# Kernel optimization log

Hardware: AMD Instinct MI355X
Metric: run time of the kernel (lower is better)

## Reference

```python
import jax, jax.numpy as jnp
from jax import lax
import numpy as np
import math

B, LBL, PRED, CIN = 16, 48, 336, 7
L = LBL + PRED
DM, E = 512, 2
DIN, N, DCONV = 2 * DM, 16, 4
DTR = math.ceil(DM / 16)  # 32
TF = 4  # freq='h' time features
EPS = 1e-5


def _ln(x, w, b):
    m = x.mean(-1, keepdims=True)
    v = ((x - m) ** 2).mean(-1, keepdims=True)
    return (x - m) / jnp.sqrt(v + EPS) * w + b


def _silu(x):
    return x * jax.nn.sigmoid(x)


def _token_embed(x, w):
    # Conv1d(c_in, d_model, k=3, padding=1, circular, bias=False). x: (B,L,C), w: (DM,C,3)
    xp = jnp.concatenate([x[:, -1:], x, x[:, :1]], axis=1)  # circular pad along L
    y = lax.conv_general_dilated(xp.transpose(0, 2, 1), w, (1,), 'VALID',
                                 dimension_numbers=('NCH', 'OIH', 'NCH'))
    return y.transpose(0, 2, 1)  # (B,L,DM)


def _selective_scan(u, dt, A, Bm, Cm):
    # u,dt: (B,L,DIN); A: (DIN,N); Bm,Cm: (B,L,N)
    h0 = jnp.zeros((u.shape[0], DIN, N), u.dtype)

    def step(h, inp):
        u_t, dt_t, B_t, C_t = inp  # (B,DIN),(B,DIN),(B,N),(B,N)
        dA = jnp.exp(dt_t[:, :, None] * A)  # (B,DIN,N)
        h = dA * h + (dt_t * u_t)[:, :, None] * B_t[:, None, :]
        y = jnp.einsum('bdn,bn->bd', h, C_t)
        return h, y

    _, ys = lax.scan(step, h0, (u.transpose(1, 0, 2), dt.transpose(1, 0, 2),
                                Bm.transpose(1, 0, 2), Cm.transpose(1, 0, 2)))
    return ys.transpose(1, 0, 2)  # (B,L,DIN)


def _mamba(x, p):
    (in_w, conv_w, conv_b, xproj_w, dtproj_w, dtproj_b, A_log, Dp, out_w) = p
    xz = x @ in_w.T                      # (B,L,2*DIN)
    xin, z = jnp.split(xz, 2, axis=-1)
    # depthwise causal conv1d, kernel DCONV
    xt = jnp.pad(xin.transpose(0, 2, 1), ((0, 0), (0, 0), (DCONV - 1, 0)))
    xc = lax.conv_general_dilated(xt, conv_w, (1,), 'VALID', feature_group_count=DIN,
                                  dimension_numbers=('NCH', 'OIH', 'NCH'))
    xc = _silu((xc + conv_b[None, :, None]).transpose(0, 2, 1))  # (B,L,DIN)
    dbc = xc @ xproj_w.T                 # (B,L,DTR+2N)
    dt_r, Bm, Cm = dbc[..., :DTR], dbc[..., DTR:DTR + N], dbc[..., DTR + N:]
    dt = jax.nn.softplus(dt_r @ dtproj_w.T + dtproj_b)  # (B,L,DIN)
    A = -jnp.exp(A_log)                  # (DIN,N)
    y = _selective_scan(xc, dt, A, Bm, Cm) + xc * Dp
    y = y * _silu(z)
    return y @ out_w.T                   # (B,L,DM)


def _model(x_dec, x_mark_dec, token_w, timef_w, layer_ps, fin_w, fin_b, out_w):
    mean = lax.stop_gradient(x_dec[:, :LBL].mean(1, keepdims=True))
    head = x_dec[:, :LBL] - mean
    std = lax.stop_gradient(jnp.sqrt(head.var(axis=1, keepdims=True) + EPS))
    head = head / std
    xd = jnp.concatenate([head, x_dec[:, LBL:]], axis=1)
    x = _token_embed(xd, token_w) + x_mark_dec @ timef_w.T  # DataEmbedding_wo_pos (eval: no dropout)
    for i in range(E):
        nw, nb = layer_ps[0][i], layer_ps[1][i]
        mp = tuple(layer_ps[j][i] for j in range(2, 11))
        x = x + _mamba(_ln(x, nw, nb), mp)
    x = _ln(x, fin_w, fin_b)
    out = x @ out_w.T
    out = out * std + mean
    return out[:, -PRED:, :]


def setup_inputs() -> dict:
    key = jax.random.key(0)
    ks = jax.random.split(key, 20)
    s = 0.02
    d = {
        'x_enc': jax.random.normal(ks[0], (B, 96, CIN), jnp.float32),
        'x_mark_enc': jax.random.normal(ks[1], (B, 96, TF), jnp.float32),
        'x_dec': jax.random.normal(ks[2], (B, L, CIN), jnp.float32),
        'x_mark_dec': jax.random.normal(ks[3], (B, L, TF), jnp.float32),
        'token_w': jax.random.normal(ks[4], (DM, CIN, 3), jnp.float32) * s,
        'timef_w': jax.random.normal(ks[5], (DM, TF), jnp.float32) * s,
        'norm_w': jnp.ones((E, DM), jnp.float32),
        'norm_b': jnp.zeros((E, DM), jnp.float32),
        'in_proj_w': jax.random.normal(ks[6], (E, 2 * DIN, DM), jnp.float32) * s,
        'conv_w': jax.random.normal(ks[7], (E, DIN, 1, DCONV), jnp.float32) * s,
        'conv_b': jnp.zeros((E, DIN), jnp.float32),
        'xproj_w': jax.random.normal(ks[8], (E, DTR + 2 * N, DIN), jnp.float32) * s,
        'dtproj_w': jax.random.normal(ks[9], (E, DIN, DTR), jnp.float32) * s,
        'dtproj_b': jnp.full((E, DIN), -4.0, jnp.float32),
        'A_log': jnp.tile(jnp.log(jnp.arange(1, N + 1, dtype=jnp.float32)), (E, DIN, 1)),
        'D': jnp.ones((E, DIN), jnp.float32),
        'outproj_w': jax.random.normal(ks[10], (E, DM, DIN), jnp.float32) * s,
        'final_norm_w': jnp.ones((DM,), jnp.float32),
        'final_norm_b': jnp.zeros((DM,), jnp.float32),
        'out_w': jax.random.normal(ks[11], (CIN, DM), jnp.float32) * s,
    }
    return d


def reference(x_enc, x_mark_enc, x_dec, x_mark_dec, token_w, timef_w, norm_w, norm_b,
              in_proj_w, conv_w, conv_b, xproj_w, dtproj_w, dtproj_b, A_log, D,
              outproj_w, final_norm_w, final_norm_b, out_w):
    layer_ps = (norm_w, norm_b, in_proj_w, conv_w, conv_b, xproj_w, dtproj_w,
                dtproj_b, A_log, D, outproj_w)
    return _model(x_dec, x_mark_dec, token_w, timef_w, layer_ps,
                  final_norm_w, final_norm_b, out_w)
```

## Files before the change

### kernel.cpp

```cpp
#include <hip/hip_runtime.h>

#define B_    16
#define LBL_  48
#define PRED_ 336
#define CIN_  7
#define L_    384
#define DM_   512
#define E_    2
#define DIN_  1024
#define N_    16
#define DCONV_ 4
#define DTR_  32
#define TF_   4
#define EPSF  1e-5f
#define NSEG  16
#define SEGL  24
#define SC2   2
#define NCHK  12

typedef unsigned short u16;
typedef __attribute__((ext_vector_type(8))) short short8;
typedef __attribute__((ext_vector_type(4))) float f32x4;

__device__ __forceinline__ float bf2f(u16 u){
  union { float f; unsigned int i; } cv; cv.i = ((unsigned int)u) << 16; return cv.f;
}
__device__ __forceinline__ u16 f2bf(float f){
  union { float f; unsigned int i; } cv; cv.f = f;
  unsigned int x = cv.i;
  unsigned int lsb = (x >> 16) & 1u;
  x += 0x7fffu + lsb;
  return (u16)(x >> 16);
}
__device__ __forceinline__ float lo16(unsigned int v){
  union { float f; unsigned int i; } cv; cv.i = v << 16; return cv.f;
}
__device__ __forceinline__ float hi16(unsigned int v){
  union { float f; unsigned int i; } cv; cv.i = v & 0xffff0000u; return cv.f;
}

#define GLDS(g, l) __builtin_amdgcn_global_load_lds( \
    (const __attribute__((address_space(1))) void*)(g), \
    (__attribute__((address_space(3))) void*)(l), 16, 0, 0)

#define PO_XDEC   0
#define PO_XMARK  43008
#define PO_TOKW   67584
#define PO_TIMEF  78336
#define PO_NORMW  80384
#define PO_NORMB  81408
#define PO_INW    82432
#define PO_CONVW  2179584
#define PO_CONVB  2187776
#define PO_XPROJ  2189824
#define PO_DTW    2320896
#define PO_DTB    2386432
#define PO_ALOG   2388480
#define PO_DP     2421248
#define PO_OUTW   2423296
#define PO_FNW    3471872
#define PO_FNB    3472384
#define PO_HEADW  3472896
#define P_TOTAL   3476480
#define A_X    3476480
#define A_LNB  6622208
#define A_XZ   9767936
#define A_DT   22350848
#define A_DBC  28642304
#define A_XD   29035520
#define A_MEAN 29078528
#define A_STD  29078640
#define A_DTR  29100032

struct Ptrs { const void* p[18]; };

__device__ __forceinline__ float wredsum(float s){
  #pragma unroll
  for (int off = 32; off; off >>= 1) s += __shfl_xor(s, off, 64);
  return s;
}

__device__ __forceinline__ void qpowers(float q, float* p){
  float q2 = q*q;
  float q4 = q2*q2;
  float q8 = q4*q4;
  float q3 = q2*q;
  p[0]=q;      p[1]=q2;     p[2]=q3;     p[3]=q4;
  p[4]=q4*q;   p[5]=q4*q2;  p[6]=q4*q3;  p[7]=q8;
  p[8]=q8*q;   p[9]=q8*q2;  p[10]=q8*q3; p[11]=q8*q4;
  p[12]=q8*p[4]; p[13]=q8*p[5]; p[14]=q8*p[6]; p[15]=q8*q8;
}

__global__ __launch_bounds__(256) void convert_kernel(Ptrs ps, float* __restrict__ dst){
  const int offs[18] = {PO_XDEC, PO_XMARK, PO_TOKW, PO_TIMEF, PO_NORMW, PO_NORMB,
                        PO_INW, PO_CONVW, PO_CONVB, PO_XPROJ, PO_DTW, PO_DTB,
                        PO_ALOG, PO_DP, PO_OUTW, PO_FNW, PO_FNB, PO_HEADW};
  int idx = blockIdx.x * 256 + threadIdx.x;
  if (idx >= P_TOTAL) return;
  int seg = 0;
  #pragma unroll
  for (int s = 1; s < 18; s++) if (idx >= offs[s]) seg = s;
  int off = idx - offs[seg];
  int isbf = (((const u16*)ps.p[4])[0] == 0x3F80u);
  if (seg == 6 || seg == 9 || seg == 10 || seg == 14){
    u16 hv = isbf ? ((const u16*)ps.p[seg])[off]
                  : f2bf(((const float*)ps.p[seg])[off]);
    ((u16*)(dst + offs[seg]))[off] = hv;
  } else {
    float v = isbf ? bf2f(((const u16*)ps.p[seg])[off])
                   : ((const float*)ps.p[seg])[off];
    dst[idx] = v;
  }
}

__global__ __launch_bounds__(64) void prep_kernel(const float* __restrict__ x_dec, float* __restrict__ xd,
                            float* __restrict__ meanv, float* __restrict__ stdv){
  int i = blockIdx.x;
  int b = i / CIN_, c = i % CIN_;
  int lane = threadIdx.x;
  float v0 = (lane < LBL_) ? x_dec[(b*L_+lane)*CIN_+c] : 0.f;
  float m = wredsum(v0) * (1.f/LBL_);
  float dv = (lane < LBL_) ? (v0 - m) : 0.f;
  float sd = sqrtf(wredsum(dv*dv) * (1.f/LBL_) + EPSF);
  if (lane == 0){ meanv[i] = m; stdv[i] = sd; }
  float inv = 1.f / sd;
  #pragma unroll
  for (int t = lane; t < L_; t += 64){
    float v = x_dec[(b*L_+t)*CIN_+c];
    xd[(b*L_+t)*CIN_+c] = (t < LBL_) ? (v - m) * inv : v;
  }
}

__global__ __launch_bounds__(256) void embed_ln_kernel(const float* __restrict__ xd,
      const float* __restrict__ token_w, const float* __restrict__ x_mark,
      const float* __restrict__ timef_w, const float* __restrict__ nw,
      const float* __restrict__ nb, float* __restrict__ x, u16* __restrict__ out){
  int tok = blockIdx.x*4 + (threadIdx.x >> 6);
  int lane = threadIdx.x & 63;
  int t = tok % L_;
  int b = tok / L_;
  int tm1 = (t == 0) ? L_-1 : t-1;
  int tp1 = (t == L_-1) ? 0 : t+1;
  const float* r0 = xd + (b*L_+tm1)*CIN_;
  const float* r1 = xd + (b*L_+t  )*CIN_;
  const float* r2 = xd + (b*L_+tp1)*CIN_;
  const float* mk = x_mark + (b*L_+t)*TF_;
  float a0[CIN_], a1[CIN_], a2[CIN_], mkv[TF_];
  #pragma unroll
  for (int ci = 0; ci < CIN_; ci++){ a0[ci]=r0[ci]; a1[ci]=r1[ci]; a2[ci]=r2[ci]; }
  #pragma unroll
  for (int f = 0; f < TF_; f++) mkv[f] = mk[f];
  float v[8];
  #pragma unroll
  for (int j = 0; j < 8; j++){
    int d = lane*8 + j;
    float acc = 0.f;
    #pragma unroll
    for (int ci = 0; ci < CIN_; ci++){
      const float* w = token_w + (d*CIN_+ci)*3;
      acc += a0[ci]*w[0] + a1[ci]*w[1] + a2[ci]*w[2];
    }
    #pragma unroll
    for (int f = 0; f < TF_; f++)
      acc += mkv[f] * timef_w[d*TF_+f];
    v[j] = acc;
  }
  float* xr = x + (size_t)tok*DM_ + lane*8;
  *(float4*)xr       = (float4){v[0],v[1],v[2],v[3]};
  *(float4*)(xr + 4) = (float4){v[4],v[5],v[6],v[7]};
  float s = (v[0]+v[1])+(v[2]+v[3])+((v[4]+v[5])+(v[6]+v[7]));
  float mean = wredsum(s) * (1.f/DM_);
  float s2 = 0.f;
  #pragma unroll
  for (int j = 0; j < 8; j++){ v[j] -= mean; s2 += v[j]*v[j]; }
  float rstd = rsqrtf(wredsum(s2) * (1.f/DM_) + EPSF);
  const float* wr = nw + lane*8;
  const float* br = nb + lane*8;
  uint4 o; unsigned int* op = (unsigned int*)&o;
  #pragma unroll
  for (int k = 0; k < 4; k++){
    u16 e0 = f2bf(v[2*k]   * rstd * wr[2*k]   + br[2*k]);
    u16 e1 = f2bf(v[2*k+1] * rstd * wr[2*k+1] + br[2*k+1]);
    op[k] = (unsigned int)e0 | ((unsigned int)e1 << 16);
  }
  *(uint4*)(out + (size_t)tok*DM_ + lane*8) = o;
}

__global__ __launch_bounds__(256) void ln_kernel(const float* __restrict__ x,
     const float* __restrict__ w, const float* __restrict__ bias, u16* __restrict__ out){
  int tok = blockIdx.x*4 + (threadIdx.x >> 6);
  int lane = threadIdx.x & 63;
  const float* xr = x + (size_t)tok*DM_ + lane*8;
  float4 a = *(const float4*)xr;
  float4 bq = *(const float4*)(xr + 4);
  float v[8] = {a.x,a.y,a.z,a.w,bq.x,bq.y,bq.z,bq.w};
  float s = (v[0]+v[1])+(v[2]+v[3])+((v[4]+v[5])+(v[6]+v[7]));
  float mean = wredsum(s) * (1.f/DM_);
  float s2 = 0.f;
  #pragma unroll
  for (int j = 0; j < 8; j++){ v[j] -= mean; s2 += v[j]*v[j]; }
  float rstd = rsqrtf(wredsum(s2) * (1.f/DM_) + EPSF);
  const float* wr = w + lane*8;
  const float* br = bias + lane*8;
  uint4 o; unsigned int* op = (unsigned int*)&o;
  #pragma unroll
  for (int k = 0; k < 4; k++){
    u16 e0 = f2bf(v[2*k]   * rstd * wr[2*k]   + br[2*k]);
    u16 e1 = f2bf(v[2*k+1] * rstd * wr[2*k+1] + br[2*k+1]);
    op[k] = (unsigned int)e0 | ((unsigned int)e1 << 16);
  }
  *(uint4*)(out + (size_t)tok*DM_ + lane*8) = o;
}

template<int TN, int ACCUM, int BF16OUT, int DTR>
__global__ __launch_bounds__(256) void gemm_mfma(const u16* __restrict__ A, const u16* __restrict__ Wt,
    void* __restrict__ C, int M, int N, int K, u16* __restrict__ dtrb){
  constexpr int WN = TN / 2;
  constexpr int NI = WN / 16;
  __shared__ u16 As[128 * 32];
  __shared__ u16 Ws[TN * 32];
  int tid = threadIdx.x;
  int wv = tid >> 6, lane = tid & 63;
  int wm = (wv & 1) * 64, wn = (wv >> 1) * WN;
  int m0 = blockIdx.y * 128, n0 = blockIdx.x * TN;
  int la = lane & 15, lk = lane >> 4;
  f32x4 acc[4][NI];
  #pragma unroll
  for (int i = 0; i < 4; i++)
    #pragma unroll
    for (int j = 0; j < NI; j++) acc[i][j] = (f32x4){0.f, 0.f, 0.f, 0.f};
  int srow = lane >> 2, scol = (lane & 3) * 8;
  const u16* Ag0 = A + (size_t)(m0 + wv*32 + srow) * K + scol;
  const u16* Ag1 = Ag0 + (size_t)16 * K;
  u16* Al0 = As + wv*1024 + lane*8;
  u16* Al1 = As + wv*1024 + 512 + lane*8;
  const u16 *Wg0, *Wg1;
  u16 *Wl0, *Wl1;
  if constexpr (TN == 128){
    Wg0 = Wt + (size_t)(n0 + wv*32 + srow) * K + scol;
    Wg1 = Wg0 + (size_t)16 * K;
    Wl0 = Ws + wv*1024 + lane*8;
    Wl1 = Ws + wv*1024 + 512 + lane*8;
  } else {
    Wg0 = Wt + (size_t)(n0 + wv*16 + srow) * K + scol;
    Wg1 = nullptr;
    Wl0 = Ws + wv*512 + lane*8;
    Wl1 = nullptr;
  }
  for (int k0 = 0; k0 < K; k0 += 32){
    GLDS(Ag0 + k0, Al0);
    GLDS(Ag1 + k0, Al1);
    GLDS(Wg0 + k0, Wl0);
    if constexpr (TN == 128) GLDS(Wg1 + k0, Wl1);
    __syncthreads();
    short8 af[4], bfr[NI];
    #pragma unroll
    for (int mi = 0; mi < 4; mi++) af[mi] = *(const short8*)&As[(wm + mi*16 + la)*32 + lk*8];
    #pragma unroll
    for (int ni = 0; ni < NI; ni++) bfr[ni] = *(const short8*)&Ws[(wn + ni*16 + la)*32 + lk*8];
    #pragma unroll
    for (int mi = 0; mi < 4; mi++)
      #pragma unroll
      for (int ni = 0; ni < NI; ni++)
        acc[mi][ni] = __builtin_amdgcn_mfma_f32_16x16x32_bf16(af[mi], bfr[ni], acc[mi][ni], 0, 0, 0);
    __syncthreads();
  }
  #pragma unroll
  for (int mi = 0; mi < 4; mi++)
    #pragma unroll
    for (int ni = 0; ni < NI; ni++){
      int row = m0 + wm + mi*16 + lk*4;
      int col = n0 + wn + ni*16 + la;
      #pragma unroll
      for (int r = 0; r < 4; r++){
        if constexpr (BF16OUT){
          u16* p = (u16*)C + (size_t)row * N + col;
          p[(size_t)r * N] = f2bf(acc[mi][ni][r]);
        } else {
          float* p = (float*)C + (size_t)row * N + col;
          if (ACCUM) p[(size_t)r * N] += acc[mi][ni][r];
          else       p[(size_t)r * N]  = acc[mi][ni][r];
        }
      }
    }
  if constexpr (DTR){
    if (wn == 0){
      #pragma unroll
      for (int mi = 0; mi < 4; mi++)
        #pragma unroll
        for (int ni = 0; ni < NI; ni++){
          int row = m0 + wm + mi*16 + lk*4;
          int col = ni*16 + la;
          #pragma unroll
          for (int r = 0; r < 4; r++)
            dtrb[(size_t)(row + r)*32 + col] = f2bf(acc[mi][ni][r]);
        }
    }
  }
}

__global__ __launch_bounds__(256) void dtproj_mfma(const u16* __restrict__ dtrb,
    const u16* __restrict__ dtwb, const float* __restrict__ dtb, u16* __restrict__ dt){
  __shared__ u16 As[128 * 32];
  __shared__ u16 Ws[64 * 32];
  int tid = threadIdx.x;
  int wv = tid >> 6, lane = tid & 63;
  int wm = (wv & 1) * 64, wn = (wv >> 1) * 32;
  int m0 = blockIdx.y * 128, n0 = blockIdx.x * 64;
  int la = lane & 15, lk = lane >> 4;
  int srow = lane >> 2, scol = (lane & 3) * 8;
  GLDS(dtrb + (size_t)(m0 + wv*32 + srow)*32 + scol,      As + wv*1024 + lane*8);
  GLDS(dtrb + (size_t)(m0 + wv*32 + 16 + srow)*32 + scol, As + wv*1024 + 512 + lane*8);
  GLDS(dtwb + (size_t)(n0 + wv*16 + srow)*32 + scol,      Ws + wv*512 + lane*8);
  __syncthreads();
  short8 af[4], bfr[2];
  #pragma unroll
  for (int mi = 0; mi < 4; mi++) af[mi] = *(const short8*)&As[(wm + mi*16 + la)*32 + lk*8];
  #pragma unroll
  for (int ni = 0; ni < 2; ni++) bfr[ni] = *(const short8*)&Ws[(wn + ni*16 + la)*32 + lk*8];
  #pragma unroll
  for (int mi = 0; mi < 4; mi++)
    #pragma unroll
    for (int ni = 0; ni < 2; ni++){
      f32x4 acc = (f32x4){0.f,0.f,0.f,0.f};
      acc = __builtin_amdgcn_mfma_f32_16x16x32_bf16(af[mi], bfr[ni], acc, 0, 0, 0);
      int row = m0 + wm + mi*16 + lk*4;
      int d   = n0 + wn + ni*16 + la;
      float bias = dtb[d];
      #pragma unroll
      for (int r = 0; r < 4; r++){
        float raw = acc[r] + bias;
        float sp = (raw > 20.f) ? raw : log1pf(__expf(raw));
        dt[(size_t)(row + r)*DIN_ + d] = f2bf(sp);
      }
    }
}

__global__ __launch_bounds__(256) void conv_silu_kernel(const u16* __restrict__ xz,
   const float* __restrict__ cw, const float* __restrict__ cb, u16* __restrict__ xcb){
  int e = blockIdx.x * 256 + threadIdx.x;
  int c8 = (e & (DIN_/8 - 1)) * 8;
  int bt = e >> 7;
  int t  = bt % L_;
  const u16* base = xz + (size_t)bt * (2*DIN_) + c8;
  uint4 tap[4];
  tap[3] = *(const uint4*)base;
  if (t >= 1) tap[2] = *(const uint4*)(base - 1*2*DIN_);
  if (t >= 2) tap[1] = *(const uint4*)(base - 2*2*DIN_);
  if (t >= 3) tap[0] = *(const uint4*)(base - 3*2*DIN_);
  float v[8];
  #pragma unroll
  for (int k = 0; k < 8; k++){
    float4 w = *(const float4*)(cw + (c8 + k)*4);
    float s = cb[c8 + k];
    #pragma unroll
    for (int j = 0; j < 4; j++){
      if (j >= 3 - t){
        const unsigned int* tp = (const unsigned int*)&tap[j];
        float xv = (k & 1) ? hi16(tp[k >> 1]) : lo16(tp[k >> 1]);
        s += xv * ((const float*)&w)[j];
      }
    }
    v[k] = s / (1.f + __expf(-s));
  }
  uint4 o;
  unsigned int* op = (unsigned int*)&o;
  #pragma unroll
  for (int k = 0; k < 4; k++)
    op[k] = (unsigned int)f2bf(v[2*k]) | ((unsigned int)f2bf(v[2*k+1]) << 16);
  *(uint4*)(xcb + (size_t)bt * DIN_ + c8) = o;
}

#define WSTR2 896
__global__ __launch_bounds__(1024, 1) void scan_kernel(
    u16* __restrict__ ub_yb,
    const float* __restrict__ dbc, const u16* __restrict__ xz,
    const u16* __restrict__ dtp,
    const float* __restrict__ A_log, const float* __restrict__ Dp){
  __shared__ float smem[16384];

  int tid = threadIdx.x;
  int lane = tid & 63;
  int seg  = tid >> 6;
  int b = blockIdx.x >> 4;
  int g = blockIdx.x & 15;
  int d = g*64 + lane;
  size_t base = (size_t)b * L_;

  float* wbase = smem + seg * WSTR2;
  float* sbc = wbase;
  float* su  = wbase + 128;
  float* sz  = wbase + 384;
  float* sdt = wbase + 640;

  int st = lane >> 5;
  int j  = lane & 31;

  float A[16];
  #pragma unroll
  for (int n = 0; n < 16; n += 4){
    float4 av = *(const float4*)(A_log + (size_t)d*N_ + n);
    A[n] = -__expf(av.x); A[n+1] = -__expf(av.y); A[n+2] = -__expf(av.z); A[n+3] = -__expf(av.w);
  }
  float Dv = Dp[d];
  bool fastA = true;
  #pragma unroll
  for (int n = 0; n < 16; n++) fastA = fastA && (fabsf(A[n] + (float)(n+1)) < 1e-3f*(n+1));

  float h[16];
  #pragma unroll
  for (int n = 0; n < 16; n++) h[n] = 0.f;

  auto ldc = [&](int c, float& kbc, unsigned int& ku, unsigned int& kz,
                 unsigned int& kt, bool wz){
    size_t tokr = base + seg*SEGL + c*SC2 + st;
    kbc = dbc[tokr*64 + 32 + j];
    ku  = ((const unsigned int*)(ub_yb + tokr*DIN_ + g*64))[j];
    kt  = ((const unsigned int*)(dtp + tokr*DIN_ + g*64))[j];
    if (wz) kz = ((const unsigned int*)(xz + tokr*(2*DIN_) + DIN_ + g*64))[j];
  };
  auto stc = [&](int buf, float kbc, unsigned int ku, unsigned int kz,
                 unsigned int kt, bool wz){
    sbc[buf*64 + st*32 + j] = kbc;
    su [buf*128 + st*64 + 2*j]     = lo16(ku);
    su [buf*128 + st*64 + 2*j + 1] = hi16(ku);
    sdt[buf*128 + st*64 + 2*j]     = lo16(kt);
    sdt[buf*128 + st*64 + 2*j + 1] = hi16(kt);
    if (wz){
      sz[buf*128 + st*64 + 2*j]     = lo16(kz);
      sz[buf*128 + st*64 + 2*j + 1] = hi16(kz);
    }
  };

  float S = 0.f;
  {
    float kbc; unsigned int ku, kz, kt;
    ldc(0, kbc, ku, kz, kt, false);
    stc(0, kbc, ku, kz, kt, false);
    for (int c = 0; c < NCHK; c++){
      int cur = c & 1;
      bool have = (c + 1 < NCHK);
      float nbc; unsigned int nu, nz, nt;
      if (have) ldc(c+1, nbc, nu, nz, nt, false);
      for (int s = 0; s < SC2; s++){
        float dtv = sdt[cur*128 + s*64 + lane];
        float u   = su [cur*128 + s*64 + lane];
        const float* bcrow = sbc + cur*64 + s*32;
        float Bf[16];
        #pragma unroll
        for (int i = 0; i < 16; i += 4){
          float4 bv = *(const float4*)(bcrow + i);
          Bf[i] = bv.x; Bf[i+1] = bv.y; Bf[i+2] = bv.z; Bf[i+3] = bv.w;
        }
        float du = dtv * u;
        S += dtv;
        if (fastA){
          float q = __expf(-dtv);
          float p[16];
          qpowers(q, p);
          #pragma unroll
          for (int n = 0; n < 16; n++) h[n] = p[n] * h[n] + du * Bf[n];
        } else {
          #pragma unroll
          for (int n = 0; n < 16; n++){
            float dA = __expf(dtv * A[n]);
            h[n] = dA * h[n] + du * Bf[n];
          }
        }
      }
      if (have) stc(1 - cur, nbc, nu, nz, nt, false);
    }
  }

  #pragma unroll
  for (int half = 0; half < 2; half++){
    __syncthreads();
    #pragma unroll
    for (int n = 0; n < 8; n++){
      int nn = half*8 + n;
      smem[(n*NSEG + seg)*64 + lane]        = h[nn];
      smem[8192 + (n*NSEG + seg)*64 + lane] = __expf(A[nn] * S);
    }
    __syncthreads();
    float hs[8];
    #pragma unroll
    for (int n = 0; n < 8; n++) hs[n] = 0.f;
    for (int jj = 0; jj < seg; jj++){
      #pragma unroll
      for (int n = 0; n < 8; n++){
        float qh = smem[(n*NSEG + jj)*64 + lane];
        float qP = smem[8192 + (n*NSEG + jj)*64 + lane];
        hs[n] = qh + qP * hs[n];
      }
    }
    #pragma unroll
    for (int n = 0; n < 8; n++) h[half*8 + n] = hs[n];
  }
  __syncthreads();

  {
    float kbc; unsigned int ku, kz, kt;
    ldc(0, kbc, ku, kz, kt, true);
    stc(0, kbc, ku, kz, kt, true);
    for (int c = 0; c < NCHK; c++){
      int cur = c & 1;
      bool have = (c + 1 < NCHK);
      float nbc; unsigned int nu, nz, nt;
      if (have) ldc(c+1, nbc, nu, nz, nt, true);
      for (int s = 0; s < SC2; s++){
        float dtv = sdt[cur*128 + s*64 + lane];
        float u   = su [cur*128 + s*64 + lane];
        float z   = sz [cur*128 + s*64 + lane];
        const float* bcrow = sbc + cur*64 + s*32;
        float Bf[16], Cf[16];
        #pragma unroll
        for (int i = 0; i < 16; i += 4){
          float4 bv = *(const float4*)(bcrow + i);
          float4 cv = *(const float4*)(bcrow + 16 + i);
          Bf[i] = bv.x; Bf[i+1] = bv.y; Bf[i+2] = bv.z; Bf[i+3] = bv.w;
          Cf[i] = cv.x; Cf[i+1] = cv.y; Cf[i+2] = cv.z; Cf[i+3] = cv.w;
        }
        float du = dtv * u;
        float acc = 0.f;
        if (fastA){
          float q = __expf(-dtv);
          float p[16];
          qpowers(q, p);
          #pragma unroll
          for (int n = 0; n < 16; n++){
            h[n] = p[n] * h[n] + du * Bf[n];
            acc += h[n] * Cf[n];
          }
        } else {
          #pragma unroll
          for (int n = 0; n < 16; n++){
            float dA = __expf(dtv * A[n]);
            h[n] = dA * h[n] + du * Bf[n];
            acc += h[n] * Cf[n];
          }
        }
        float y = acc + u * Dv;
        size_t tok = base + seg*SEGL + c*SC2 + s;
        ub_yb[tok*DIN_ + d] = f2bf(y * (z / (1.f + __expf(-z))));
      }
      if (have) stc(1 - cur, nbc, nu, nz, nt, true);
    }
  }
}

__global__ __launch_bounds__(256) void head_kernel(const float* __restrict__ x,
    const float* __restrict__ fw, const float* __restrict__ fb, const float* __restrict__ ow,
    const float* __restrict__ meanv, const float* __restrict__ stdv, void* __restrict__ out,
    const u16* __restrict__ dtype_probe){
  int wav = blockIdx.x*4 + (threadIdx.x >> 6);
  int lane = threadIdx.x & 63;
  if (wav >= B_*PRED_) return;
  int b = wav / PRED_;
  int tt = wav % PRED_;
  int tok = b*L_ + LBL_ + tt;
  const float* xr = x + (size_t)tok*DM_ + lane*8;
  float4 a = *(const float4*)xr;
  float4 bq = *(const float4*)(xr + 4);
  float v[8] = {a.x,a.y,a.z,a.w,bq.x,bq.y,bq.z,bq.w};
  float s = (v[0]+v[1])+(v[2]+v[3])+((v[4]+v[5])+(v[6]+v[7]));
  float mean = wredsum(s) * (1.f/DM_);
  float s2 = 0.f;
  #pragma unroll
  for (int j = 0; j < 8; j++){ v[j] -= mean; s2 += v[j]*v[j]; }
  float rstd = rsqrtf(wredsum(s2) * (1.f/DM_) + EPSF);
  const float* fwr = fw + lane*8;
  const float* fbr = fb + lane*8;
  #pragma unroll
  for (int j = 0; j < 8; j++) v[j] = v[j] * rstd * fwr[j] + fbr[j];
  int isbf = (dtype_probe[0] == 0x3F80u);
  for (int o = 0; o < CIN_; o++){
    const float* owr = ow + (size_t)o*DM_ + lane*8;
    float part = 0.f;
    #pragma unroll
    for (int j = 0; j < 8; j++) part += v[j] * owr[j];
    part = wredsum(part);
    if (lane == 0){
      float res = part * stdv[b*CIN_ + o] + meanv[b*CIN_ + o];
      size_t oidx = (size_t)(b*PRED_ + tt)*CIN_ + o;
      if (isbf) ((u16*)out)[oidx] = f2bf(res);
      else      ((float*)out)[oidx] = res;
    }
  }
}

extern "C" void kernel_launch(void* const* d_in, const int* in_sizes, int n_in,
                              void* d_out, int out_size, void* d_ws, size_t ws_size,
                              hipStream_t stream){
  float* P = (float*)d_ws;

  Ptrs ps;
  for (int i = 0; i < 18; i++) ps.p[i] = d_in[2 + i];

  float* x    = P + A_X;
  u16*   lnxb = (u16*)(P + A_LNB);
  u16*   xcb  = (u16*)(P + A_LNB);
  u16*   xz   = (u16*)(P + A_XZ);
  u16*   dt   = (u16*)(P + A_DT);
  u16*   dtrb = (u16*)(P + A_DTR);
  float* dbc  = P + A_DBC;
  float* xd   = P + A_XD;
  float* meanv= P + A_MEAN;
  float* stdv = P + A_STD;
  const u16* bwi = (const u16*)(P + PO_INW);
  const u16* bwx = (const u16*)(P + PO_XPROJ);
  const u16* bwd = (const u16*)(P + PO_DTW);
  const u16* bwo = (const u16*)(P + PO_OUTW);

  convert_kernel<<<(P_TOTAL+255)/256, 256, 0, stream>>>(ps, P);
  prep_kernel<<<B_*CIN_, 64, 0, stream>>>(P + PO_XDEC, xd, meanv, stdv);
  embed_ln_kernel<<<(B_*L_)/4, 256, 0, stream>>>(
      xd, P + PO_TOKW, P + PO_XMARK, P + PO_TIMEF,
      P + PO_NORMW, P + PO_NORMB, x, lnxb);

  for (int e = 0; e < E_; e++){
    if (e > 0)
      ln_kernel<<<(B_*L_)/4, 256, 0, stream>>>(x, P + PO_NORMW + e*DM_, P + PO_NORMB + e*DM_, lnxb);
    gemm_mfma<128,0,1,0><<<dim3((2*DIN_)/128, (B_*L_)/128), 256, 0, stream>>>(
        lnxb, bwi + (size_t)e*2*DIN_*DM_, xz, B_*L_, 2*DIN_, DM_, nullptr);
    conv_silu_kernel<<<(B_*L_*DIN_)/(256*8), 256, 0, stream>>>(
        xz, P + PO_CONVW + e*DIN_*DCONV_, P + PO_CONVB + e*DIN_, xcb);
    gemm_mfma<64,0,0,1><<<dim3(1, (B_*L_)/128), 256, 0, stream>>>(
        xcb, bwx + (size_t)e*64*DIN_, dbc, B_*L_, 64, DIN_, dtrb);
    dtproj_mfma<<<dim3(DIN_/64, (B_*L_)/128), 256, 0, stream>>>(
        dtrb, bwd + (size_t)e*DIN_*DTR_, P + PO_DTB + e*DIN_, dt);
    scan_kernel<<<256, 1024, 0, stream>>>(
        xcb, dbc, xz, dt, P + PO_ALOG + e*DIN_*N_, P + PO_DP + e*DIN_);
    gemm_mfma<64,1,0,0><<<dim3(DM_/64, (B_*L_)/128), 256, 0, stream>>>(
        xcb, bwo + (size_t)e*DM_*DIN_, x, B_*L_, DM_, DIN_, nullptr);
  }

  head_kernel<<<(B_*PRED_+3)/4, 256, 0, stream>>>(
      x, P + PO_FNW, P + PO_FNB, P + PO_HEADW, meanv, stdv, d_out, (const u16*)d_in[6]);
}
```

Baseline: 452.3 us.

## Split x_proj GEMM over K into four partial slices and deepen GEMM K tile

```diff
diff --git a/kernel.cpp b/kernel.cpp
--- a/kernel.cpp
+++ b/kernel.cpp
@@ -70,7 +70,8 @@
 #define A_XD   29035520
 #define A_MEAN 29078528
 #define A_STD  29078640
-#define A_DTR  29100032
+#define A_DBC4 16059392
+#define DBC_SL ((size_t)(B_*L_)*64)
 
 struct Ptrs { const void* p[18]; };
 
@@ -212,13 +213,13 @@
   *(uint4*)(out + (size_t)tok*DM_ + lane*8) = o;
 }
 
-template<int TN, int ACCUM, int BF16OUT, int DTR>
+template<int TN, int ACCUM, int BF16OUT>
 __global__ __launch_bounds__(256) void gemm_mfma(const u16* __restrict__ A, const u16* __restrict__ Wt,
-    void* __restrict__ C, int M, int N, int K, u16* __restrict__ dtrb){
+    void* __restrict__ C, int M, int N, int K){
   constexpr int WN = TN / 2;
   constexpr int NI = WN / 16;
-  __shared__ u16 As[128 * 32];
-  __shared__ u16 Ws[TN * 32];
+  __shared__ u16 As[128 * 64];
+  __shared__ u16 Ws[TN * 64];
   int tid = threadIdx.x;
   int wv = tid >> 6, lane = tid & 63;
   int wm = (wv & 1) * 64, wn = (wv >> 1) * WN;
@@ -229,40 +230,41 @@
   for (int i = 0; i < 4; i++)
     #pragma unroll
     for (int j = 0; j < NI; j++) acc[i][j] = (f32x4){0.f, 0.f, 0.f, 0.f};
-  int srow = lane >> 2, scol = (lane & 3) * 8;
-  const u16* Ag0 = A + (size_t)(m0 + wv*32 + srow) * K + scol;
-  const u16* Ag1 = Ag0 + (size_t)16 * K;
-  u16* Al0 = As + wv*1024 + lane*8;
-  u16* Al1 = As + wv*1024 + 512 + lane*8;
-  const u16 *Wg0, *Wg1;
-  u16 *Wl0, *Wl1;
+  int sr = lane >> 3, sc = (lane & 7) * 8;
+  const u16* Ag = A + (size_t)(m0 + wv*32 + sr) * K + sc;
+  u16* Al = As + (wv*32)*64 + lane*8;
+  const u16 *Wg; u16 *Wl;
   if constexpr (TN == 128){
-    Wg0 = Wt + (size_t)(n0 + wv*32 + srow) * K + scol;
-    Wg1 = Wg0 + (size_t)16 * K;
-    Wl0 = Ws + wv*1024 + lane*8;
-    Wl1 = Ws + wv*1024 + 512 + lane*8;
+    Wg = Wt + (size_t)(n0 + wv*32 + sr) * K + sc;
+    Wl = Ws + (wv*32)*64 + lane*8;
   } else {
-    Wg0 = Wt + (size_t)(n0 + wv*16 + srow) * K + scol;
-    Wg1 = nullptr;
-    Wl0 = Ws + wv*512 + lane*8;
-    Wl1 = nullptr;
-  }
-  for (int k0 = 0; k0 < K; k0 += 32){
-    GLDS(Ag0 + k0, Al0);
-    GLDS(Ag1 + k0, Al1);
-    GLDS(Wg0 + k0, Wl0);
-    if constexpr (TN == 128) GLDS(Wg1 + k0, Wl1);
+    Wg = Wt + (size_t)(n0 + wv*16 + sr) * K + sc;
+    Wl = Ws + (wv*16)*64 + lane*8;
+  }
+  for (int k0 = 0; k0 < K; k0 += 64){
+    #pragma unroll
+    for (int i = 0; i < 4; i++) GLDS(Ag + (size_t)(i*8)*K + k0, Al + i*512);
+    if constexpr (TN == 128){
+      #pragma unroll
+      for (int i = 0; i < 4; i++) GLDS(Wg + (size_t)(i*8)*K + k0, Wl + i*512);
+    } else {
+      #pragma unroll
+      for (int i = 0; i < 2; i++) GLDS(Wg + (size_t)(i*8)*K + k0, Wl + i*512);
+    }
     __syncthreads();
-    short8 af[4], bfr[NI];
-    #pragma unroll
-    for (int mi = 0; mi < 4; mi++) af[mi] = *(const short8*)&As[(wm + mi*16 + la)*32 + lk*8];
-    #pragma unroll
-    for (int ni = 0; ni < NI; ni++) bfr[ni] = *(const short8*)&Ws[(wn + ni*16 + la)*32 + lk*8];
-    #pragma unroll
-    for (int mi = 0; mi < 4; mi++)
-      #pragma unroll
-      for (int ni = 0; ni < NI; ni++)
-        acc[mi][ni] = __builtin_amdgcn_mfma_f32_16x16x32_bf16(af[mi], bfr[ni], acc[mi][ni], 0, 0, 0);
+    #pragma unroll
+    for (int ks = 0; ks < 2; ks++){
+      short8 af[4], bfr[NI];
+      #pragma unroll
+      for (int mi = 0; mi < 4; mi++) af[mi] = *(const short8*)&As[(wm + mi*16 + la)*64 + ks*32 + lk*8];
+      #pragma unroll
+      for (int ni = 0; ni < NI; ni++) bfr[ni] = *(const short8*)&Ws[(wn + ni*16 + la)*64 + ks*32 + lk*8];
+      #pragma unroll
+      for (int mi = 0; mi < 4; mi++)
+        #pragma unroll
+        for (int ni = 0; ni < NI; ni++)
+          acc[mi][ni] = __builtin_amdgcn_mfma_f32_16x16x32_bf16(af[mi], bfr[ni], acc[mi][ni], 0, 0, 0);
+    }
     __syncthreads();
   }
   #pragma unroll
@@ -283,23 +285,60 @@
         }
       }
     }
-  if constexpr (DTR){
-    if (wn == 0){
+}
+
+__global__ __launch_bounds__(256) void xproj_mfma(const u16* __restrict__ A, const u16* __restrict__ Wt,
+    float* __restrict__ out4){
+  __shared__ u16 As[128 * 64];
+  __shared__ u16 Ws[64 * 64];
+  int tid = threadIdx.x;
+  int wv = tid >> 6, lane = tid & 63;
+  int wm = (wv & 1) * 64, wn = (wv >> 1) * 32;
+  int m0 = blockIdx.y * 128;
+  int kc = blockIdx.x;
+  int la = lane & 15, lk = lane >> 4;
+  f32x4 acc[4][2];
+  #pragma unroll
+  for (int i = 0; i < 4; i++){ acc[i][0] = (f32x4){0.f,0.f,0.f,0.f}; acc[i][1] = (f32x4){0.f,0.f,0.f,0.f}; }
+  int sr = lane >> 3, sc = (lane & 7) * 8;
+  const u16* Ag = A + (size_t)(m0 + wv*32 + sr) * DIN_ + kc*256 + sc;
+  u16* Al = As + (wv*32)*64 + lane*8;
+  const u16* Wg = Wt + (size_t)(wv*16 + sr) * DIN_ + kc*256 + sc;
+  u16* Wl = Ws + (wv*16)*64 + lane*8;
+  for (int k0 = 0; k0 < 256; k0 += 64){
+    #pragma unroll
+    for (int i = 0; i < 4; i++) GLDS(Ag + (size_t)(i*8)*DIN_ + k0, Al + i*512);
+    #pragma unroll
+    for (int i = 0; i < 2; i++) GLDS(Wg + (size_t)(i*8)*DIN_ + k0, Wl + i*512);
+    __syncthreads();
+    #pragma unroll
+    for (int ks = 0; ks < 2; ks++){
+      short8 af[4], bfr[2];
+      #pragma unroll
+      for (int mi = 0; mi < 4; mi++) af[mi] = *(const short8*)&As[(wm + mi*16 + la)*64 + ks*32 + lk*8];
+      #pragma unroll
+      for (int ni = 0; ni < 2; ni++) bfr[ni] = *(const short8*)&Ws[(wn + ni*16 + la)*64 + ks*32 + lk*8];
       #pragma unroll
       for (int mi = 0; mi < 4; mi++)
         #pragma unroll
-        for (int ni = 0; ni < NI; ni++){
-          int row = m0 + wm + mi*16 + lk*4;
-          int col = ni*16 + la;
-          #pragma unroll
-          for (int r = 0; r < 4; r++)
-            dtrb[(size_t)(row + r)*32 + col] = f2bf(acc[mi][ni][r]);
-        }
-    }
-  }
-}
-
-__global__ __launch_bounds__(256) void dtproj_mfma(const u16* __restrict__ dtrb,
+        for (int ni = 0; ni < 2; ni++)
+          acc[mi][ni] = __builtin_amdgcn_mfma_f32_16x16x32_bf16(af[mi], bfr[ni], acc[mi][ni], 0, 0, 0);
+    }
+    __syncthreads();
+  }
+  #pragma unroll
+  for (int mi = 0; mi < 4; mi++)
+    #pragma unroll
+    for (int ni = 0; ni < 2; ni++){
+      int row = m0 + wm + mi*16 + lk*4;
+      int col = wn + ni*16 + la;
+      #pragma unroll
+      for (int r = 0; r < 4; r++)
+        out4[((size_t)kc*(B_*L_) + row + r)*64 + col] = acc[mi][ni][r];
+    }
+}
+
+__global__ __launch_bounds__(256) void dtproj_mfma(const float* __restrict__ dbc4,
     const u16* __restrict__ dtwb, const float* __restrict__ dtb, u16* __restrict__ dt){
   __shared__ u16 As[128 * 32];
   __shared__ u16 Ws[64 * 32];
@@ -309,9 +348,20 @@
   int m0 = blockIdx.y * 128, n0 = blockIdx.x * 64;
   int la = lane & 15, lk = lane >> 4;
   int srow = lane >> 2, scol = (lane & 3) * 8;
-  GLDS(dtrb + (size_t)(m0 + wv*32 + srow)*32 + scol,      As + wv*1024 + lane*8);
-  GLDS(dtrb + (size_t)(m0 + wv*32 + 16 + srow)*32 + scol, As + wv*1024 + 512 + lane*8);
-  GLDS(dtwb + (size_t)(n0 + wv*16 + srow)*32 + scol,      Ws + wv*512 + lane*8);
+  #pragma unroll
+  for (int i = 0; i < 8; i++){
+    int idx = i*512 + tid*2;
+    int row = idx >> 5, col = idx & 31;
+    const float* p = dbc4 + (size_t)(m0 + row)*64 + col;
+    float s0 = 0.f, s1 = 0.f;
+    #pragma unroll
+    for (int k = 0; k < 4; k++){
+      s0 += p[(size_t)k*DBC_SL];
+      s1 += p[(size_t)k*DBC_SL + 1];
+    }
+    *(unsigned int*)&As[row*32 + col] = (unsigned int)f2bf(s0) | ((unsigned int)f2bf(s1) << 16);
+  }
+  GLDS(dtwb + (size_t)(n0 + wv*16 + srow)*32 + scol, Ws + wv*512 + lane*8);
   __syncthreads();
   short8 af[4], bfr[2];
   #pragma unroll
@@ -414,7 +464,8 @@
   auto ldc = [&](int c, float& kbc, unsigned int& ku, unsigned int& kz,
                  unsigned int& kt, bool wz){
     size_t tokr = base + seg*SEGL + c*SC2 + st;
-    kbc = dbc[tokr*64 + 32 + j];
+    const float* pb = dbc + tokr*64 + 32 + j;
+    kbc = (pb[0] + pb[DBC_SL]) + (pb[2*DBC_SL] + pb[3*DBC_SL]);
     ku  = ((const unsigned int*)(ub_yb + tokr*DIN_ + g*64))[j];
     kt  = ((const unsigned int*)(dtp + tokr*DIN_ + g*64))[j];
     if (wz) kz = ((const unsigned int*)(xz + tokr*(2*DIN_) + DIN_ + g*64))[j];
@@ -601,8 +652,7 @@
   u16*   xcb  = (u16*)(P + A_LNB);
   u16*   xz   = (u16*)(P + A_XZ);
   u16*   dt   = (u16*)(P + A_DT);
-  u16*   dtrb = (u16*)(P + A_DTR);
-  float* dbc  = P + A_DBC;
+  float* dbc4 = P + A_DBC4;
   float* xd   = P + A_XD;
   float* meanv= P + A_MEAN;
   float* stdv = P + A_STD;
@@ -620,18 +670,18 @@
   for (int e = 0; e < E_; e++){
     if (e > 0)
       ln_kernel<<<(B_*L_)/4, 256, 0, stream>>>(x, P + PO_NORMW + e*DM_, P + PO_NORMB + e*DM_, lnxb);
-    gemm_mfma<128,0,1,0><<<dim3((2*DIN_)/128, (B_*L_)/128), 256, 0, stream>>>(
-        lnxb, bwi + (size_t)e*2*DIN_*DM_, xz, B_*L_, 2*DIN_, DM_, nullptr);
+    gemm_mfma<128,0,1><<<dim3((2*DIN_)/128, (B_*L_)/128), 256, 0, stream>>>(
+        lnxb, bwi + (size_t)e*2*DIN_*DM_, xz, B_*L_, 2*DIN_, DM_);
     conv_silu_kernel<<<(B_*L_*DIN_)/(256*8), 256, 0, stream>>>(
         xz, P + PO_CONVW + e*DIN_*DCONV_, P + PO_CONVB + e*DIN_, xcb);
-    gemm_mfma<64,0,0,1><<<dim3(1, (B_*L_)/128), 256, 0, stream>>>(
-        xcb, bwx + (size_t)e*64*DIN_, dbc, B_*L_, 64, DIN_, dtrb);
+    xproj_mfma<<<dim3(4, (B_*L_)/128), 256, 0, stream>>>(
+        xcb, bwx + (size_t)e*64*DIN_, dbc4);
     dtproj_mfma<<<dim3(DIN_/64, (B_*L_)/128), 256, 0, stream>>>(
-        dtrb, bwd + (size_t)e*DIN_*DTR_, P + PO_DTB + e*DIN_, dt);
+        dbc4, bwd + (size_t)e*DIN_*DTR_, P + PO_DTB + e*DIN_, dt);
     scan_kernel<<<256, 1024, 0, stream>>>(
-        xcb, dbc, xz, dt, P + PO_ALOG + e*DIN_*N_, P + PO_DP + e*DIN_);
-    gemm_mfma<64,1,0,0><<<dim3(DM_/64, (B_*L_)/128), 256, 0, stream>>>(
-        xcb, bwo + (size_t)e*DM_*DIN_, x, B_*L_, DM_, DIN_, nullptr);
+        xcb, dbc4, xz, dt, P + PO_ALOG + e*DIN_*N_, P + PO_DP + e*DIN_);
+    gemm_mfma<64,1,0><<<dim3(DM_/64, (B_*L_)/128), 256, 0, stream>>>(
+        xcb, bwo + (size_t)e*DM_*DIN_, x, B_*L_, DM_, DIN_);
   }
 
   head_kernel<<<(B_*PRED_+3)/4, 256, 0, stream>>>(
```

After: 440.5 us. 1.03x faster.
